# Optimization experiments

Hardware: AMD Instinct MI355X
Metric: run time of the kernel (lower is better)

Reference implementation:

```python
import jax, jax.numpy as jnp
from jax import lax
import numpy as np

PRE_NMS_TOPN = 2000
POST_NMS_TOPN = 300
NMS_IOU_THRESHOLD = 0.7
EPS = 1e-8


def setup_inputs() -> dict:
    key = jax.random.key(0)
    k1, k2 = jax.random.split(key, 2)
    B, H, W, A = 64, 100, 100, 9
    # small-magnitude deltas so exp(dh/dw) stays sane, as real RPN outputs do
    rpn_bbox_deltas = jax.random.normal(k1, (B, H, W, A * 4), dtype=jnp.float32) * 0.1
    rpn_labels = jax.random.uniform(k2, (B, H, W, A), dtype=jnp.float32)
    # grid anchors, normalized coords, 3 scales x 3 ratios = 9 per position
    ys = (jnp.arange(H, dtype=jnp.float32) + 0.5) / H
    xs = (jnp.arange(W, dtype=jnp.float32) + 0.5) / W
    scales = jnp.array([0.1, 0.2, 0.4], dtype=jnp.float32)
    ratios = jnp.array([0.5, 1.0, 2.0], dtype=jnp.float32)
    hh = (scales[:, None] * jnp.sqrt(ratios)[None, :]).reshape(-1)  # [9]
    ww = (scales[:, None] / jnp.sqrt(ratios)[None, :]).reshape(-1)  # [9]
    cy, cx = jnp.meshgrid(ys, xs, indexing="ij")  # [H,W]
    cy, cx = cy[..., None], cx[..., None]         # [H,W,1]
    anchors = jnp.stack(
        [cy - hh / 2, cx - ww / 2, cy + hh / 2, cx + ww / 2], axis=-1
    ).reshape(-1, 4)  # [H*W*9, 4] = [90000, 4]
    return {"rpn_bbox_deltas": rpn_bbox_deltas, "rpn_labels": rpn_labels, "anchors": anchors}


def _decode_deltas(anchors, deltas):
    # anchors [N,4] (y1,x1,y2,x2), deltas [B,N,4] (dy,dx,dh,dw)
    anc_h = anchors[:, 2] - anchors[:, 0]
    anc_w = anchors[:, 3] - anchors[:, 1]
    anc_cy = anchors[:, 0] + 0.5 * anc_h
    anc_cx = anchors[:, 1] + 0.5 * anc_w
    h = jnp.exp(deltas[..., 2]) * anc_h
    w = jnp.exp(deltas[..., 3]) * anc_w
    cy = deltas[..., 0] * anc_h + anc_cy
    cx = deltas[..., 1] * anc_w + anc_cx
    y1 = cy - 0.5 * h
    x1 = cx - 0.5 * w
    return jnp.stack([y1, x1, y1 + h, x1 + w], axis=-1)  # [B,N,4]


def _nms_single(boxes):
    # boxes [PRE,4] already sorted by score descending; greedy hard NMS
    n = boxes.shape[0]
    area = jnp.maximum(boxes[:, 2] - boxes[:, 0], 0.0) * jnp.maximum(boxes[:, 3] - boxes[:, 1], 0.0)
    idx = jnp.arange(n)

    def body(i, keep):
        b = boxes[i]
        yy1 = jnp.maximum(b[0], boxes[:, 0])
        xx1 = jnp.maximum(b[1], boxes[:, 1])
        yy2 = jnp.minimum(b[2], boxes[:, 2])
        xx2 = jnp.minimum(b[3], boxes[:, 3])
        inter = jnp.maximum(yy2 - yy1, 0.0) * jnp.maximum(xx2 - xx1, 0.0)
        iou = inter / (area[i] + area - inter + EPS)
        suppress = (iou > NMS_IOU_THRESHOLD) & (idx > i) & keep[i]
        return keep & ~suppress

    keep = lax.fori_loop(0, n, body, jnp.ones((n,), dtype=bool))
    # compact kept boxes (score order) into fixed [POST,4], zero-padded
    pos = jnp.where(keep, jnp.cumsum(keep) - 1, POST_NMS_TOPN)
    pos = jnp.minimum(pos, POST_NMS_TOPN)
    out = jnp.zeros((POST_NMS_TOPN + 1, 4), dtype=boxes.dtype).at[pos].set(boxes)[:POST_NMS_TOPN]
    return jnp.clip(out, 0.0, 1.0)  # clip_boxes=True in tf combined NMS


def reference(rpn_bbox_deltas, rpn_labels, anchors):
    B = rpn_bbox_deltas.shape[0]
    N = anchors.shape[0]
    deltas = rpn_bbox_deltas.reshape(B, N, 4)
    labels = rpn_labels.reshape(B, N)
    boxes = _decode_deltas(anchors, deltas)             # [B,N,4]
    _, pre_idx = lax.top_k(labels, PRE_NMS_TOPN)        # [B,PRE] sorted desc
    pre_boxes = jnp.take_along_axis(boxes, pre_idx[..., None], axis=1)  # [B,PRE,4]
    roi_bboxes = jax.vmap(_nms_single)(pre_boxes)       # [B,POST,4]
    return lax.stop_gradient(roi_bboxes)
```

## Files before the change

### kernel.cpp

```cpp
#include <hip/hip_runtime.h>
#include <stdint.h>


#define PRE 2000
#define POST 300
#define TILE 512
#define IOU_THR 0.7f
#define EPSV 1e-8f
#define SORTN 2048
#define NBINS 2048
#define CANDCAP 512
#define CONS 1984
#define SL 8
#define KBUF 1536

typedef unsigned long long u64;

__device__ __forceinline__ uint32_t flip_f32(uint32_t b) {
    return b ^ ((uint32_t)((int32_t)b >> 31) | 0x80000000u);
}

__device__ __forceinline__ int bin_of(float s) {
    int bn = (int)(s * 2048.0f);
    return min(max(bn, 0), NBINS - 1);
}

__device__ __forceinline__ u64 make_key(float s, int idx, int bn) {
    uint32_t ub = flip_f32(__float_as_uint(s));
    return ((u64)ub << 32) | ((uint32_t)bn << 20) |
           (uint32_t)(0xFFFFF - idx);
}

__device__ __forceinline__ bool iou_gt(const float4& bi, float ai,
                                       const float4& bj, float aj) {
    float yy1 = fmaxf(bi.x, bj.x);
    float xx1 = fmaxf(bi.y, bj.y);
    float yy2 = fminf(bi.z, bj.z);
    float xx2 = fminf(bi.w, bj.w);
    float inter = fmaxf(yy2 - yy1, 0.f) * fmaxf(xx2 - xx1, 0.f);
    float iou = inter / (ai + aj - inter + EPSV);
    return iou > IOU_THR;
}

__device__ __forceinline__ float area_of(const float4& bx) {
    return fmaxf(bx.z - bx.x, 0.f) * fmaxf(bx.w - bx.y, 0.f);
}

__device__ __forceinline__ u64 cs_keep(u64 v, u64 pv, int i, int j, int k) {
    bool lower   = ((i & j) == 0);
    bool desc    = ((i & k) == 0);
    bool keepmax = (desc == lower);
    u64 mx = v > pv ? v : pv;
    u64 mn = v > pv ? pv : v;
    return keepmax ? mx : mn;
}

__global__ __launch_bounds__(256) void k1_hist_gather(
    const float4* __restrict__ score4,
    uint32_t* __restrict__ g_hist,
    u64*      __restrict__ g_pairs,
    int*      __restrict__ g_scnt,
    int N)
{
    const int blk = blockIdx.x;
    const int b   = blk / SL;
    const int s   = blk % SL;
    const int tid = threadIdx.x;
    const int F4PB = N >> 2;
    const int F4PS = (F4PB + SL - 1) / SL;

    __shared__ uint32_t hist[NBINS];
    __shared__ u64 keybuf[KBUF];
    __shared__ int kcnt;

    for (int i = tid; i < NBINS; i += 256) hist[i] = 0u;
    if (tid == 0) kcnt = 0;
    __syncthreads();

    const float4* src = score4 + (size_t)b * F4PB;
    const int n0 = s * F4PS, n1 = min(n0 + F4PS, F4PB);
    for (int n = n0 + tid; n < n1; n += 256) {
        float4 v = src[n];
        float sv[4] = {v.x, v.y, v.z, v.w};
#pragma unroll
        for (int c = 0; c < 4; ++c) {
            int bn = bin_of(sv[c]);
            atomicAdd(&hist[bn], 1u);
            if (bn >= CONS) {
                int q = atomicAdd(&kcnt, 1);
                if (q < KBUF) keybuf[q] = make_key(sv[c], 4 * n + c, bn);
            }
        }
    }
    __syncthreads();

    uint32_t* gh = g_hist + ((size_t)b * SL + s) * NBINS;
    for (int i = tid; i < NBINS; i += 256) gh[i] = hist[i];

    if (tid == 0) g_scnt[b * SL + s] = kcnt;
    int lc = min(kcnt, KBUF);
    u64* gp = g_pairs + ((size_t)b * SL + s) * KBUF;
    for (int i = tid; i < lc; i += 256) gp[i] = keybuf[i];
}

__global__ __launch_bounds__(1024) void k2_sort(
    const float4* __restrict__ score4,
    const u64*  __restrict__ g_pairs,
    const int*  __restrict__ g_scnt,
    const uint32_t* __restrict__ g_hist,
    u64* __restrict__ g_sorted,
    int N)
{
    const int b    = blockIdx.x;
    const int tid  = threadIdx.x;
    const int lane = tid & 63;
    const int wv   = tid >> 6;

    __shared__ u64 pairs[SORTN];
    __shared__ u64 cand[CANDCAP];
    __shared__ uint32_t wtot[16];
    __shared__ int segbase[64];
    __shared__ int segcnt[64];
    __shared__ uint32_t cur[64];
    __shared__ int sh_bsel, sh_tprime, sh_cnt, sh_nc, sh_flag, sh_big;
    __shared__ uint32_t sh_pivot;

    const int F4PB = N >> 2;

    uint32_t* hist = (uint32_t*)pairs;
    {
        const uint32_t* gh = g_hist + (size_t)b * SL * NBINS;
#pragma unroll
        for (int h = 0; h < 2; ++h) {
            int i = tid + h * 1024;
            uint32_t acc = 0u;
#pragma unroll
            for (int s = 0; s < SL; ++s) acc += gh[(size_t)s * NBINS + i];
            hist[i] = acc;
        }
    }
    if (tid < 64) cur[tid] = 0u;
    if (tid == 0) {
        sh_cnt = 0; sh_nc = 0; sh_big = 0;
        int f = 0;
#pragma unroll
        for (int s = 0; s < SL; ++s)
            if (g_scnt[b * SL + s] > KBUF) f = 1;
        sh_flag = f;
    }
    __syncthreads();

    {
        const int i0 = wv * 128 + lane;
        const int i1 = i0 + 64;
        int h0 = (int)hist[i0];
        int h1 = (int)hist[i1];
        int s0 = h0, s1 = h1;
#pragma unroll
        for (int off = 1; off < 64; off <<= 1) {
            int t0 = __shfl_down(s0, off, 64);
            int t1 = __shfl_down(s1, off, 64);
            if (lane + off < 64) { s0 += t0; s1 += t1; }
        }
        int sum_h1 = __shfl(s1, 0, 64);
        if (lane == 0) wtot[wv] = (uint32_t)(__shfl(s0, 0, 64) + sum_h1);
        __syncthreads();
        int offtot = 0;
        for (int w2 = wv + 1; w2 < 16; ++w2) offtot += (int)wtot[w2];
        int S0 = s0 + sum_h1 + offtot;
        int S1 = s1 + offtot;
        if (S0 >= PRE && S0 - h0 < PRE) { sh_bsel = i0; sh_tprime = PRE - (S0 - h0); }
        if (S1 >= PRE && S1 - h1 < PRE) { sh_bsel = i1; sh_tprime = PRE - (S1 - h1); }
        if (i1 >= CONS) {
            segbase[i1 - CONS] = S1 - h1;
            segcnt [i1 - CONS] = h1;
        }
    }
    __syncthreads();
    const int bsel   = sh_bsel;
    const int tprime = sh_tprime;
    bool flag = (bsel < CONS) || sh_flag;
    if (!flag && segcnt[bsel - CONS] > CANDCAP) flag = true;
    __syncthreads();

    if (!flag) {
        for (int s = 0; s < SL; ++s) {
            const int  cs = min(g_scnt[b * SL + s], KBUF);
            const u64* gp = g_pairs + ((size_t)b * SL + s) * KBUF;
            for (int i = tid; i < cs; i += 1024) {
                u64 key = gp[i];
                int bn = (int)((key >> 20) & 0xFFFu);
                if (bn > bsel) {
                    int c = (int)atomicAdd(&cur[bn - CONS], 1u);
                    pairs[segbase[bn - CONS] + c] = key;
                } else if (bn == bsel) {
                    int t = atomicAdd(&sh_nc, 1);
                    if (t < CANDCAP) cand[t] = key;
                }
            }
        }
        __syncthreads();
        const int nc = min(sh_nc, CANDCAP);
        for (int i = tid; i < nc; i += 1024) {
            uint32_t vi = (uint32_t)(cand[i] >> 32);
            int g = 0, e = 0;
            for (int j = 0; j < nc; ++j) {
                uint32_t vj = (uint32_t)(cand[j] >> 32);
                g += (vj > vi);
                e += (vj == vi);
            }
            if (g < tprime && g + e >= tprime) sh_pivot = vi;
        }
        __syncthreads();
        const uint32_t pivot = sh_pivot;
        for (int i = tid; i < nc; i += 1024) {
            uint32_t vi = (uint32_t)(cand[i] >> 32);
            if (vi >= pivot) {
                int c = (int)atomicAdd(&cur[bsel - CONS], 1u);
                pairs[segbase[bsel - CONS] + c] = cand[i];
            }
        }
        __syncthreads();
        const int total = segbase[bsel - CONS] + (int)cur[bsel - CONS];
        for (int q = total + tid; q < SORTN; q += 1024) pairs[q] = 0ull;
        if (tid < 64 && (int)cur[tid] > 128) sh_big = 1;
        __syncthreads();
    } else {
        const float4* src = score4 + (size_t)b * F4PB;
        for (int n = tid; n < F4PB; n += 1024) {
            float4 v = src[n];
            float sv[4] = {v.x, v.y, v.z, v.w};
#pragma unroll
            for (int c = 0; c < 4; ++c) {
                int bn = bin_of(sv[c]);
                if (bn >= bsel) {
                    u64 key = make_key(sv[c], 4 * n + c, bn);
                    if (bn > bsel) {
                        int q = atomicAdd(&sh_cnt, 1);
                        if (q < SORTN) pairs[q] = key;
                    } else {
                        int t = atomicAdd(&sh_nc, 1);
                        if (t < CANDCAP) cand[t] = key;
                    }
                }
            }
        }
        __syncthreads();
        const int nc = min(sh_nc, CANDCAP);
        for (int i = tid; i < nc; i += 1024) {
            uint32_t vi = (uint32_t)(cand[i] >> 32);
            int g = 0, e = 0;
            for (int j = 0; j < nc; ++j) {
                uint32_t vj = (uint32_t)(cand[j] >> 32);
                g += (vj > vi);
                e += (vj == vi);
            }
            if (g < tprime && g + e >= tprime) sh_pivot = vi;
        }
        __syncthreads();
        const uint32_t pivot = sh_pivot;
        for (int i = tid; i < nc; i += 1024) {
            uint32_t vi = (uint32_t)(cand[i] >> 32);
            if (vi >= pivot) {
                int q = atomicAdd(&sh_cnt, 1);
                if (q < SORTN) pairs[q] = cand[i];
            }
        }
        __syncthreads();
        const int total = min(sh_cnt, SORTN);
        for (int q = total + tid; q < SORTN; q += 1024) pairs[q] = 0ull;
        if (tid == 0) sh_big = 1;
        __syncthreads();
    }

    if (!sh_big) {
        for (int sgi = wv; sgi < 64; sgi += 16) {
            int n = (int)cur[sgi];
            if (n <= 0) continue;
            int base = segbase[sgi];
            if (n <= 64) {
                u64 e = (lane < n) ? pairs[base + lane] : 0ull;
#pragma unroll
                for (int k = 2; k <= 64; k <<= 1)
                    for (int j = k >> 1; j > 0; j >>= 1)
                        e = cs_keep(e, __shfl_xor(e, j, 64), lane, j, k);
                if (lane < n) pairs[base + lane] = e;
            } else {
                u64 e0 = (lane < n) ? pairs[base + lane] : 0ull;
                u64 e1 = (lane + 64 < n) ? pairs[base + lane + 64] : 0ull;
#pragma unroll
                for (int k = 2; k <= 128; k <<= 1) {
                    for (int j = k >> 1; j > 0; j >>= 1) {
                        if (j == 64) {
                            u64 a = e0, c = e1;
                            e0 = cs_keep(a, c, lane, 64, k);
                            e1 = cs_keep(c, a, lane + 64, 64, k);
                        } else {
                            e0 = cs_keep(e0, __shfl_xor(e0, j, 64), lane, j, k);
                            e1 = cs_keep(e1, __shfl_xor(e1, j, 64), lane + 64, j, k);
                        }
                    }
                }
                if (lane < n) pairs[base + lane] = e0;
                if (lane + 64 < n) pairs[base + lane + 64] = e1;
            }
        }
        __syncthreads();
        g_sorted[(size_t)b * SORTN + tid]        = pairs[tid];
        g_sorted[(size_t)b * SORTN + tid + 1024] = pairs[tid + 1024];
    } else {
        const int i0 = wv * 128 + lane;
        const int i1 = i0 + 64;
        u64 e0 = pairs[i0];
        u64 e1 = pairs[i1];
        for (int k = 2; k <= SORTN; k <<= 1) {
            for (int j = k >> 1; j > 0; j >>= 1) {
                if (j >= 128) {
                    pairs[i0] = e0;
                    pairs[i1] = e1;
                    __syncthreads();
                    u64 p0 = pairs[i0 ^ j];
                    u64 p1 = pairs[i1 ^ j];
                    __syncthreads();
                    e0 = cs_keep(e0, p0, i0, j, k);
                    e1 = cs_keep(e1, p1, i1, j, k);
                } else if (j == 64) {
                    u64 a = e0, c = e1;
                    e0 = cs_keep(a, c, i0, 64, k);
                    e1 = cs_keep(c, a, i1, 64, k);
                } else {
                    e0 = cs_keep(e0, __shfl_xor(e0, j, 64), i0, j, k);
                    e1 = cs_keep(e1, __shfl_xor(e1, j, 64), i1, j, k);
                }
            }
        }
        g_sorted[(size_t)b * SORTN + i0] = e0;
        g_sorted[(size_t)b * SORTN + i1] = e1;
    }
}

__global__ __launch_bounds__(256) void k3_decode(
    const float4* __restrict__ deltas,
    const float4* __restrict__ anchors,
    const u64*  __restrict__ g_sorted,
    float4* __restrict__ g_boxes,
    float*  __restrict__ g_area,
    int N)
{
    const int b   = blockIdx.x >> 2;
    const int s   = blockIdx.x & 3;
    const int tid = threadIdx.x;
    const int r0 = s * 512, r1 = min(r0 + 512, PRE);

    const float4* dl = deltas + (size_t)b * N;
    for (int r = r0 + tid; r < r1; r += 256) {
        u64 key = g_sorted[(size_t)b * SORTN + r];
        uint32_t idx = 0xFFFFFu - (uint32_t)(key & 0xFFFFFull);
        float4 bx = make_float4(0.f, 0.f, 0.f, 0.f);
        float  ar = 0.f;
        if (idx < (uint32_t)N) {
            float4 d  = dl[idx];
            float4 an = anchors[idx];
            float ah  = an.z - an.x;
            float aw  = an.w - an.y;
            float acy = an.x + 0.5f * ah;
            float acx = an.y + 0.5f * aw;
            float h   = expf(d.z) * ah;
            float w   = expf(d.w) * aw;
            float cy  = d.x * ah + acy;
            float cx  = d.y * aw + acx;
            float y1  = cy - 0.5f * h;
            float x1  = cx - 0.5f * w;
            bx = make_float4(y1, x1, y1 + h, x1 + w);
            ar = fmaxf(bx.z - bx.x, 0.f) * fmaxf(bx.w - bx.y, 0.f);
        }
        g_boxes[(size_t)b * PRE + r] = bx;
        g_area [(size_t)b * PRE + r] = ar;
    }
}

__global__ __launch_bounds__(256) void k4_supmat(
    const float4* __restrict__ g_boxes,
    uint32_t* __restrict__ g_supmat,
    uint32_t* __restrict__ g_supT)
{
    const int b   = blockIdx.x >> 4;
    const int s   = blockIdx.x & 15;
    const int tid = threadIdx.x;

    __shared__ float4 box[TILE];
    for (int i = tid; i < TILE; i += 256)
        box[i] = g_boxes[(size_t)b * PRE + i];
    __syncthreads();

    const int rbase = s * 32;
#pragma unroll
    for (int k = 0; k < 2; ++k) {
        int idx = tid + k * 256;
        int row = rbase + (idx & 31);
        int w   = idx >> 5;
        int jbase = w << 5;
        float4 bi = box[row];
        float  ai = area_of(bi);
        uint32_t bits = 0u;
        if (jbase + 31 > row) {
#pragma unroll
            for (int c = 0; c < 32; ++c) {
                int j = jbase + c;
                float4 bj = box[j];
                float  aj = area_of(bj);
                bool gt = (j > row) & iou_gt(bi, ai, bj, aj);
                bits |= ((uint32_t)gt) << c;
            }
        }
        g_supmat[((size_t)b * TILE + row) * 16 + w] = bits;
    }

    if (s < 8 && tid < 128) {
        int q  = s;
        int j  = tid >> 1;
        int w2 = tid & 1;
        int C  = q * 64 + j;
        float4 bc = box[C];
        float  ac = area_of(bc);
        uint32_t bits = 0u;
#pragma unroll
        for (int c = 0; c < 32; ++c) {
            int R = q * 64 + w2 * 32 + c;
            float4 br = box[R];
            float  ar = area_of(br);
            bool gt = (R < C) & iou_gt(br, ar, bc, ac);
            bits |= ((uint32_t)gt) << c;
        }
        g_supT[((size_t)b * TILE + C) * 2 + w2] = bits;
    }
}

__global__ __launch_bounds__(64) void k5_sweep(
    const uint32_t* __restrict__ g_supmat,
    const u64*    __restrict__ g_supT64,
    const float4* __restrict__ g_boxes,
    const float*  __restrict__ g_area,
    float4* __restrict__ out)
{
    const int b    = blockIdx.x;
    const int lane = threadIdx.x;

    __shared__ uint32_t kept[POST];
    __shared__ u64 sh_keepbits[TILE / 64];
    __shared__ uint32_t fmask[(PRE - TILE + 31) / 32];
    __shared__ int sh_kc;

    const u64* tdbase = g_supT64 + (size_t)b * TILE;

    uint32_t removedw = 0u;
    int kc = 0, nq = 0;
    u64 cw_cur = tdbase[lane];
    for (int q = 0; q < TILE / 64; ++q) {
        u64 cw_next = (q < TILE / 64 - 1) ? tdbase[(q + 1) * 64 + lane] : 0ull;
        const int cbase = q << 6;
        uint32_t rlo = (uint32_t)__builtin_amdgcn_readlane((int)removedw, 2 * q);
        uint32_t rhi = (uint32_t)__builtin_amdgcn_readlane((int)removedw, 2 * q + 1);
        u64 avail = ~(((u64)rhi << 32) | rlo);
        u64 K = 0ull;
        while (avail) {
            int i = __ffsll((long long)avail) - 1;
            K |= (1ull << i);
            u64 supp = __ballot(((cw_cur >> i) & 1ull) != 0ull);
            avail &= ~(supp | (1ull << i));
        }
        if (lane == 0) sh_keepbits[q] = K;
        kc += __popcll(K);
        nq = q + 1;
        if (kc >= POST) break;
        if (K) {
            const int w = lane & 15;
            const int g = lane >> 4;
            const uint32_t* gs =
                g_supmat + ((size_t)b * TILE + cbase + g * 16) * 16 + w;
            uint32_t acc = 0u;
#pragma unroll
            for (int r = 0; r < 16; ++r)
                if ((K >> (g * 16 + r)) & 1ull) acc |= gs[(size_t)r * 16];
            acc |= (uint32_t)__shfl_xor((int)acc, 16, 64);
            acc |= (uint32_t)__shfl_xor((int)acc, 32, 64);
            if (lane < 16) removedw |= acc;
        }
        cw_cur = cw_next;
    }
    {
        int base = 0;
        for (int q = 0; q < nq; ++q) {
            u64 kbq = sh_keepbits[q];
            int pos = base + __popcll(kbq & ((1ull << lane) - 1));
            if (((kbq >> lane) & 1ull) && pos < POST)
                kept[pos] = (uint32_t)(q * 64 + lane);
            base += __popcll(kbq);
        }
        if (lane == 0) sh_kc = min(kc, POST);
    }
    __syncthreads();
    int kcf = sh_kc;

    if (kcf < POST) {
        for (int w = lane; w < (PRE - TILE + 31) / 32; w += 64) fmask[w] = 0u;
        __syncthreads();
        for (int j = TILE + lane; j < PRE; j += 64) {
            float4 bj = g_boxes[(size_t)b * PRE + j];
            float  aj = g_area [(size_t)b * PRE + j];
            bool supd = false;
            for (int k = 0; k < kcf; ++k) {
                int i = (int)kept[k];
                float4 bi = g_boxes[(size_t)b * PRE + i];
                float  ai = g_area [(size_t)b * PRE + i];
                if (iou_gt(bi, ai, bj, aj)) { supd = true; break; }
            }
            if (supd) atomicOr(&fmask[(j - TILE) >> 5], 1u << ((j - TILE) & 31));
        }
        __syncthreads();
        int i = TILE;
        while (i < PRE && kcf < POST) {
            while (i < PRE && ((fmask[(i - TILE) >> 5] >> ((i - TILE) & 31)) & 1u)) ++i;
            if (i >= PRE) break;
            if (lane == 0) kept[kcf] = (uint32_t)i;
            ++kcf;
            if (kcf >= POST) break;
            float4 bi = g_boxes[(size_t)b * PRE + i];
            float  ai = g_area [(size_t)b * PRE + i];
            for (int j = i + 1 + lane; j < PRE; j += 64) {
                float4 bj = g_boxes[(size_t)b * PRE + j];
                float  aj = g_area [(size_t)b * PRE + j];
                if (iou_gt(bi, ai, bj, aj))
                    atomicOr(&fmask[(j - TILE) >> 5], 1u << ((j - TILE) & 31));
            }
            ++i;
            __syncthreads();
        }
    }
    __syncthreads();

    float4* ob = out + (size_t)b * POST;
    for (int r = lane; r < POST; r += 64) {
        float4 o = make_float4(0.f, 0.f, 0.f, 0.f);
        if (r < kcf) {
            float4 bx = g_boxes[(size_t)b * PRE + kept[r]];
            o.x = fminf(fmaxf(bx.x, 0.f), 1.f);
            o.y = fminf(fmaxf(bx.y, 0.f), 1.f);
            o.z = fminf(fmaxf(bx.z, 0.f), 1.f);
            o.w = fminf(fmaxf(bx.w, 0.f), 1.f);
        }
        ob[r] = o;
    }
}

extern "C" void kernel_launch(void* const* d_in, const int* in_sizes, int n_in,
                              void* d_out, int out_size, void* d_ws, size_t ws_size,
                              hipStream_t stream) {
    const float4* deltas  = (const float4*)d_in[0];
    const float*  labels  = (const float*)d_in[1];
    const float4* anchors = (const float4*)d_in[2];
    const float4* score4  = (const float4*)labels;
    float4*       outp    = (float4*)d_out;
    const int N = in_sizes[2] / 4;
    const int B = in_sizes[1] / N;

    char* ws = (char*)d_ws;
    const size_t SZ_BOXES  = (size_t)B * PRE * 16;
    const size_t SZ_PAIRS  = (size_t)B * SL * KBUF * 8;
    const size_t SZ_SORTED = (size_t)B * SORTN * 8;
    const size_t SZ_SUPMAT = (size_t)B * TILE * 16 * 4;
    const size_t SZ_SUPT   = (size_t)B * TILE * 8;
    const size_t SZ_AREA   = (size_t)B * PRE * 4;
    const size_t SZ_HIST   = (size_t)B * SL * NBINS * 4;
    float4*   g_boxes  = (float4*)ws;
    u64*      g_pairs  = (u64*)(ws + SZ_BOXES);
    u64*      g_sorted = (u64*)(ws + SZ_BOXES + SZ_PAIRS);
    uint32_t* g_supmat = (uint32_t*)(ws + SZ_BOXES + SZ_PAIRS + SZ_SORTED);
    uint32_t* g_supT   = (uint32_t*)(ws + SZ_BOXES + SZ_PAIRS + SZ_SORTED + SZ_SUPMAT);
    float*    g_area   = (float*)(ws + SZ_BOXES + SZ_PAIRS + SZ_SORTED + SZ_SUPMAT + SZ_SUPT);
    uint32_t* g_hist   = (uint32_t*)(ws + SZ_BOXES + SZ_PAIRS + SZ_SORTED + SZ_SUPMAT + SZ_SUPT + SZ_AREA);
    int*      g_scnt   = (int*)((char*)g_hist + SZ_HIST);

    k1_hist_gather<<<B * SL, 256, 0, stream>>>(score4, g_hist, g_pairs,
                                               g_scnt, N);
    k2_sort<<<B, 1024, 0, stream>>>(score4, g_pairs, g_scnt, g_hist,
                                    g_sorted, N);
    k3_decode<<<B * 4, 256, 0, stream>>>(deltas, anchors, g_sorted,
                                         g_boxes, g_area, N);
    k4_supmat<<<B * 16, 256, 0, stream>>>(g_boxes, g_supmat, g_supT);
    k5_sweep<<<B, 64, 0, stream>>>(g_supmat, (const u64*)g_supT,
                                   g_boxes, g_area, outp);
}
```

Measured before the change: 93.06 us.

## Fuse decode and diagonal suppression tiles into sort kernel, drop global histograms

Stops building the full 2048-bin histogram in the gather kernel and instead builds a 64-bin histogram from the gathered top-bin keys inside the sort kernel. All keys in the top bins are sorted by segment (total up to 4096), and a full histogram with rescan is kept only as a fallback. Box decode and the diagonal-block transposed suppression bits are fused into the sort kernel through shared memory, which removes one launch and the g_sorted and g_hist global round trips. The gather now uses more slices with smaller buffers. The trade-off is more shared memory and work in a single 1024-thread block per batch, which runs only 64 blocks.

```diff
diff --git a/kernel.cpp b/kernel.cpp
--- a/kernel.cpp
+++ b/kernel.cpp
@@ -9,10 +9,11 @@
 #define EPSV 1e-8f
 #define SORTN 2048
 #define NBINS 2048
+#define DESTCAP 4096
 #define CANDCAP 512
 #define CONS 1984
-#define SL 8
-#define KBUF 1536
+#define SL 16
+#define KBUF 768
 
 typedef unsigned long long u64;
 
@@ -55,11 +56,10 @@
     return keepmax ? mx : mn;
 }
 
-__global__ __launch_bounds__(256) void k1_hist_gather(
+__global__ __launch_bounds__(256) void k1_gather(
     const float4* __restrict__ score4,
-    uint32_t* __restrict__ g_hist,
-    u64*      __restrict__ g_pairs,
-    int*      __restrict__ g_scnt,
+    u64* __restrict__ g_pairs,
+    int* __restrict__ g_scnt,
     int N)
 {
     const int blk = blockIdx.x;
@@ -69,11 +69,9 @@
     const int F4PB = N >> 2;
     const int F4PS = (F4PB + SL - 1) / SL;
 
-    __shared__ uint32_t hist[NBINS];
     __shared__ u64 keybuf[KBUF];
     __shared__ int kcnt;
 
-    for (int i = tid; i < NBINS; i += 256) hist[i] = 0u;
     if (tid == 0) kcnt = 0;
     __syncthreads();
 
@@ -85,7 +83,6 @@
 #pragma unroll
         for (int c = 0; c < 4; ++c) {
             int bn = bin_of(sv[c]);
-            atomicAdd(&hist[bn], 1u);
             if (bn >= CONS) {
                 int q = atomicAdd(&kcnt, 1);
                 if (q < KBUF) keybuf[q] = make_key(sv[c], 4 * n + c, bn);
@@ -93,9 +90,6 @@
         }
     }
     __syncthreads();
-
-    uint32_t* gh = g_hist + ((size_t)b * SL + s) * NBINS;
-    for (int i = tid; i < NBINS; i += 256) gh[i] = hist[i];
 
     if (tid == 0) g_scnt[b * SL + s] = kcnt;
     int lc = min(kcnt, KBUF);
@@ -107,8 +101,11 @@
     const float4* __restrict__ score4,
     const u64*  __restrict__ g_pairs,
     const int*  __restrict__ g_scnt,
-    const uint32_t* __restrict__ g_hist,
-    u64* __restrict__ g_sorted,
+    const float4* __restrict__ deltas,
+    const float4* __restrict__ anchors,
+    float4* __restrict__ g_boxes,
+    float*  __restrict__ g_area,
+    uint32_t* __restrict__ g_supT,
     int N)
 {
     const int b    = blockIdx.x;
@@ -116,178 +113,78 @@
     const int lane = tid & 63;
     const int wv   = tid >> 6;
 
-    __shared__ u64 pairs[SORTN];
+    __shared__ u64 dest[DESTCAP];
+    __shared__ float4 sbox[TILE];
     __shared__ u64 cand[CANDCAP];
+    __shared__ uint32_t hist64[64];
+    __shared__ int segbase64[64];
+    __shared__ uint32_t cur64[64];
+    __shared__ int scnt_s[SL];
     __shared__ uint32_t wtot[16];
-    __shared__ int segbase[64];
-    __shared__ int segcnt[64];
-    __shared__ uint32_t cur[64];
-    __shared__ int sh_bsel, sh_tprime, sh_cnt, sh_nc, sh_flag, sh_big;
+    __shared__ int sh_flag, sh_total, sh_bsel, sh_tprime, sh_cnt, sh_nc;
     __shared__ uint32_t sh_pivot;
 
     const int F4PB = N >> 2;
 
-    uint32_t* hist = (uint32_t*)pairs;
+    if (tid < SL) scnt_s[tid] = g_scnt[b * SL + tid];
+    if (tid < 64) { hist64[tid] = 0u; cur64[tid] = 0u; }
+    if (tid == 0) { sh_flag = 0; sh_cnt = 0; sh_nc = 0; }
+    __syncthreads();
+
     {
-        const uint32_t* gh = g_hist + (size_t)b * SL * NBINS;
-#pragma unroll
-        for (int h = 0; h < 2; ++h) {
-            int i = tid + h * 1024;
-            uint32_t acc = 0u;
-#pragma unroll
-            for (int s = 0; s < SL; ++s) acc += gh[(size_t)s * NBINS + i];
-            hist[i] = acc;
-        }
-    }
-    if (tid < 64) cur[tid] = 0u;
-    if (tid == 0) {
-        sh_cnt = 0; sh_nc = 0; sh_big = 0;
-        int f = 0;
-#pragma unroll
-        for (int s = 0; s < SL; ++s)
-            if (g_scnt[b * SL + s] > KBUF) f = 1;
-        sh_flag = f;
-    }
-    __syncthreads();
-
-    {
-        const int i0 = wv * 128 + lane;
-        const int i1 = i0 + 64;
-        int h0 = (int)hist[i0];
-        int h1 = (int)hist[i1];
-        int s0 = h0, s1 = h1;
+        int raw = scnt_s[wv];
+        if (raw > KBUF) sh_flag = 1;
+        int cs = min(raw, KBUF);
+        const u64* gp = g_pairs + ((size_t)b * SL + wv) * KBUF;
+        for (int i = lane; i < cs; i += 64) {
+            int b64 = (int)((gp[i] >> 20) & 0xFFFu) - CONS;
+            atomicAdd(&hist64[b64], 1u);
+        }
+    }
+    __syncthreads();
+
+    if (wv == 0) {
+        int h = (int)hist64[lane];
+        int ssum = h;
 #pragma unroll
         for (int off = 1; off < 64; off <<= 1) {
-            int t0 = __shfl_down(s0, off, 64);
-            int t1 = __shfl_down(s1, off, 64);
-            if (lane + off < 64) { s0 += t0; s1 += t1; }
-        }
-        int sum_h1 = __shfl(s1, 0, 64);
-        if (lane == 0) wtot[wv] = (uint32_t)(__shfl(s0, 0, 64) + sum_h1);
-        __syncthreads();
-        int offtot = 0;
-        for (int w2 = wv + 1; w2 < 16; ++w2) offtot += (int)wtot[w2];
-        int S0 = s0 + sum_h1 + offtot;
-        int S1 = s1 + offtot;
-        if (S0 >= PRE && S0 - h0 < PRE) { sh_bsel = i0; sh_tprime = PRE - (S0 - h0); }
-        if (S1 >= PRE && S1 - h1 < PRE) { sh_bsel = i1; sh_tprime = PRE - (S1 - h1); }
-        if (i1 >= CONS) {
-            segbase[i1 - CONS] = S1 - h1;
-            segcnt [i1 - CONS] = h1;
-        }
-    }
-    __syncthreads();
-    const int bsel   = sh_bsel;
-    const int tprime = sh_tprime;
-    bool flag = (bsel < CONS) || sh_flag;
-    if (!flag && segcnt[bsel - CONS] > CANDCAP) flag = true;
-    __syncthreads();
+            int t = __shfl_down(ssum, off, 64);
+            if (lane + off < 64) ssum += t;
+        }
+        segbase64[lane] = ssum - h;
+        if (lane == 0) sh_total = ssum;
+        if (h > 128) sh_flag = 1;
+    }
+    __syncthreads();
+    const int total = sh_total;
+    if (tid == 0 && (total < PRE || total > DESTCAP)) sh_flag = 1;
+    __syncthreads();
+    const bool flag = (sh_flag != 0);
 
     if (!flag) {
-        for (int s = 0; s < SL; ++s) {
-            const int  cs = min(g_scnt[b * SL + s], KBUF);
-            const u64* gp = g_pairs + ((size_t)b * SL + s) * KBUF;
-            for (int i = tid; i < cs; i += 1024) {
-                u64 key = gp[i];
-                int bn = (int)((key >> 20) & 0xFFFu);
-                if (bn > bsel) {
-                    int c = (int)atomicAdd(&cur[bn - CONS], 1u);
-                    pairs[segbase[bn - CONS] + c] = key;
-                } else if (bn == bsel) {
-                    int t = atomicAdd(&sh_nc, 1);
-                    if (t < CANDCAP) cand[t] = key;
-                }
-            }
-        }
-        __syncthreads();
-        const int nc = min(sh_nc, CANDCAP);
-        for (int i = tid; i < nc; i += 1024) {
-            uint32_t vi = (uint32_t)(cand[i] >> 32);
-            int g = 0, e = 0;
-            for (int j = 0; j < nc; ++j) {
-                uint32_t vj = (uint32_t)(cand[j] >> 32);
-                g += (vj > vi);
-                e += (vj == vi);
-            }
-            if (g < tprime && g + e >= tprime) sh_pivot = vi;
-        }
-        __syncthreads();
-        const uint32_t pivot = sh_pivot;
-        for (int i = tid; i < nc; i += 1024) {
-            uint32_t vi = (uint32_t)(cand[i] >> 32);
-            if (vi >= pivot) {
-                int c = (int)atomicAdd(&cur[bsel - CONS], 1u);
-                pairs[segbase[bsel - CONS] + c] = cand[i];
-            }
-        }
-        __syncthreads();
-        const int total = segbase[bsel - CONS] + (int)cur[bsel - CONS];
-        for (int q = total + tid; q < SORTN; q += 1024) pairs[q] = 0ull;
-        if (tid < 64 && (int)cur[tid] > 128) sh_big = 1;
-        __syncthreads();
-    } else {
-        const float4* src = score4 + (size_t)b * F4PB;
-        for (int n = tid; n < F4PB; n += 1024) {
-            float4 v = src[n];
-            float sv[4] = {v.x, v.y, v.z, v.w};
-#pragma unroll
-            for (int c = 0; c < 4; ++c) {
-                int bn = bin_of(sv[c]);
-                if (bn >= bsel) {
-                    u64 key = make_key(sv[c], 4 * n + c, bn);
-                    if (bn > bsel) {
-                        int q = atomicAdd(&sh_cnt, 1);
-                        if (q < SORTN) pairs[q] = key;
-                    } else {
-                        int t = atomicAdd(&sh_nc, 1);
-                        if (t < CANDCAP) cand[t] = key;
-                    }
-                }
-            }
-        }
-        __syncthreads();
-        const int nc = min(sh_nc, CANDCAP);
-        for (int i = tid; i < nc; i += 1024) {
-            uint32_t vi = (uint32_t)(cand[i] >> 32);
-            int g = 0, e = 0;
-            for (int j = 0; j < nc; ++j) {
-                uint32_t vj = (uint32_t)(cand[j] >> 32);
-                g += (vj > vi);
-                e += (vj == vi);
-            }
-            if (g < tprime && g + e >= tprime) sh_pivot = vi;
-        }
-        __syncthreads();
-        const uint32_t pivot = sh_pivot;
-        for (int i = tid; i < nc; i += 1024) {
-            uint32_t vi = (uint32_t)(cand[i] >> 32);
-            if (vi >= pivot) {
-                int q = atomicAdd(&sh_cnt, 1);
-                if (q < SORTN) pairs[q] = cand[i];
-            }
-        }
-        __syncthreads();
-        const int total = min(sh_cnt, SORTN);
-        for (int q = total + tid; q < SORTN; q += 1024) pairs[q] = 0ull;
-        if (tid == 0) sh_big = 1;
-        __syncthreads();
-    }
-
-    if (!sh_big) {
+        int cs = min(scnt_s[wv], KBUF);
+        const u64* gp = g_pairs + ((size_t)b * SL + wv) * KBUF;
+        for (int i = lane; i < cs; i += 64) {
+            u64 key = gp[i];
+            int b64 = (int)((key >> 20) & 0xFFFu) - CONS;
+            int c = (int)atomicAdd(&cur64[b64], 1u);
+            dest[segbase64[b64] + c] = key;
+        }
+        __syncthreads();
         for (int sgi = wv; sgi < 64; sgi += 16) {
-            int n = (int)cur[sgi];
+            int n = (int)cur64[sgi];
             if (n <= 0) continue;
-            int base = segbase[sgi];
+            int base = segbase64[sgi];
             if (n <= 64) {
-                u64 e = (lane < n) ? pairs[base + lane] : 0ull;
+                u64 e = (lane < n) ? dest[base + lane] : 0ull;
 #pragma unroll
                 for (int k = 2; k <= 64; k <<= 1)
                     for (int j = k >> 1; j > 0; j >>= 1)
                         e = cs_keep(e, __shfl_xor(e, j, 64), lane, j, k);
-                if (lane < n) pairs[base + lane] = e;
+                if (lane < n) dest[base + lane] = e;
             } else {
-                u64 e0 = (lane < n) ? pairs[base + lane] : 0ull;
-                u64 e1 = (lane + 64 < n) ? pairs[base + lane + 64] : 0ull;
+                u64 e0 = (lane < n) ? dest[base + lane] : 0ull;
+                u64 e1 = (lane + 64 < n) ? dest[base + lane + 64] : 0ull;
 #pragma unroll
                 for (int k = 2; k <= 128; k <<= 1) {
                     for (int j = k >> 1; j > 0; j >>= 1) {
@@ -301,60 +198,129 @@
                         }
                     }
                 }
-                if (lane < n) pairs[base + lane] = e0;
-                if (lane + 64 < n) pairs[base + lane + 64] = e1;
-            }
-        }
-        __syncthreads();
-        g_sorted[(size_t)b * SORTN + tid]        = pairs[tid];
-        g_sorted[(size_t)b * SORTN + tid + 1024] = pairs[tid + 1024];
+                if (lane < n) dest[base + lane] = e0;
+                if (lane + 64 < n) dest[base + lane + 64] = e1;
+            }
+        }
+        __syncthreads();
     } else {
-        const int i0 = wv * 128 + lane;
-        const int i1 = i0 + 64;
-        u64 e0 = pairs[i0];
-        u64 e1 = pairs[i1];
-        for (int k = 2; k <= SORTN; k <<= 1) {
-            for (int j = k >> 1; j > 0; j >>= 1) {
-                if (j >= 128) {
-                    pairs[i0] = e0;
-                    pairs[i1] = e1;
-                    __syncthreads();
-                    u64 p0 = pairs[i0 ^ j];
-                    u64 p1 = pairs[i1 ^ j];
-                    __syncthreads();
-                    e0 = cs_keep(e0, p0, i0, j, k);
-                    e1 = cs_keep(e1, p1, i1, j, k);
-                } else if (j == 64) {
-                    u64 a = e0, c = e1;
-                    e0 = cs_keep(a, c, i0, 64, k);
-                    e1 = cs_keep(c, a, i1, 64, k);
-                } else {
-                    e0 = cs_keep(e0, __shfl_xor(e0, j, 64), i0, j, k);
-                    e1 = cs_keep(e1, __shfl_xor(e1, j, 64), i1, j, k);
+        uint32_t* hist = (uint32_t*)sbox;
+        hist[tid] = 0u; hist[tid + 1024] = 0u;
+        if (tid == 0) { sh_cnt = 0; sh_nc = 0; }
+        __syncthreads();
+        const float4* src = score4 + (size_t)b * F4PB;
+        for (int n = tid; n < F4PB; n += 1024) {
+            float4 v = src[n];
+            atomicAdd(&hist[bin_of(v.x)], 1u);
+            atomicAdd(&hist[bin_of(v.y)], 1u);
+            atomicAdd(&hist[bin_of(v.z)], 1u);
+            atomicAdd(&hist[bin_of(v.w)], 1u);
+        }
+        __syncthreads();
+        {
+            const int i0 = wv * 128 + lane;
+            const int i1 = i0 + 64;
+            int h0 = (int)hist[i0];
+            int h1 = (int)hist[i1];
+            int s0 = h0, s1 = h1;
+#pragma unroll
+            for (int off = 1; off < 64; off <<= 1) {
+                int t0 = __shfl_down(s0, off, 64);
+                int t1 = __shfl_down(s1, off, 64);
+                if (lane + off < 64) { s0 += t0; s1 += t1; }
+            }
+            int sum_h1 = __shfl(s1, 0, 64);
+            if (lane == 0) wtot[wv] = (uint32_t)(__shfl(s0, 0, 64) + sum_h1);
+            __syncthreads();
+            int offtot = 0;
+            for (int w2 = wv + 1; w2 < 16; ++w2) offtot += (int)wtot[w2];
+            int S0 = s0 + sum_h1 + offtot;
+            int S1 = s1 + offtot;
+            if (S0 >= PRE && S0 - h0 < PRE) { sh_bsel = i0; sh_tprime = PRE - (S0 - h0); }
+            if (S1 >= PRE && S1 - h1 < PRE) { sh_bsel = i1; sh_tprime = PRE - (S1 - h1); }
+        }
+        __syncthreads();
+        const int bsel   = sh_bsel;
+        const int tprime = sh_tprime;
+        __syncthreads();
+        for (int n = tid; n < F4PB; n += 1024) {
+            float4 v = src[n];
+            float sv[4] = {v.x, v.y, v.z, v.w};
+#pragma unroll
+            for (int c = 0; c < 4; ++c) {
+                int bn = bin_of(sv[c]);
+                if (bn >= bsel) {
+                    u64 key = make_key(sv[c], 4 * n + c, bn);
+                    if (bn > bsel) {
+                        int q = atomicAdd(&sh_cnt, 1);
+                        if (q < SORTN) dest[q] = key;
+                    } else {
+                        int t = atomicAdd(&sh_nc, 1);
+                        if (t < CANDCAP) cand[t] = key;
+                    }
                 }
             }
         }
-        g_sorted[(size_t)b * SORTN + i0] = e0;
-        g_sorted[(size_t)b * SORTN + i1] = e1;
-    }
-}
-
-__global__ __launch_bounds__(256) void k3_decode(
-    const float4* __restrict__ deltas,
-    const float4* __restrict__ anchors,
-    const u64*  __restrict__ g_sorted,
-    float4* __restrict__ g_boxes,
-    float*  __restrict__ g_area,
-    int N)
-{
-    const int b   = blockIdx.x >> 2;
-    const int s   = blockIdx.x & 3;
-    const int tid = threadIdx.x;
-    const int r0 = s * 512, r1 = min(r0 + 512, PRE);
+        __syncthreads();
+        const int nc = min(sh_nc, CANDCAP);
+        for (int i = tid; i < nc; i += 1024) {
+            uint32_t vi = (uint32_t)(cand[i] >> 32);
+            int g = 0, e = 0;
+            for (int j = 0; j < nc; ++j) {
+                uint32_t vj = (uint32_t)(cand[j] >> 32);
+                g += (vj > vi);
+                e += (vj == vi);
+            }
+            if (g < tprime && g + e >= tprime) sh_pivot = vi;
+        }
+        __syncthreads();
+        const uint32_t pivot = sh_pivot;
+        for (int i = tid; i < nc; i += 1024) {
+            uint32_t vi = (uint32_t)(cand[i] >> 32);
+            if (vi >= pivot) {
+                int q = atomicAdd(&sh_cnt, 1);
+                if (q < SORTN) dest[q] = cand[i];
+            }
+        }
+        __syncthreads();
+        const int tt = min(sh_cnt, SORTN);
+        for (int q = tt + tid; q < SORTN; q += 1024) dest[q] = 0ull;
+        __syncthreads();
+        {
+            const int i0 = wv * 128 + lane;
+            const int i1 = i0 + 64;
+            u64 e0 = dest[i0];
+            u64 e1 = dest[i1];
+            for (int k = 2; k <= SORTN; k <<= 1) {
+                for (int j = k >> 1; j > 0; j >>= 1) {
+                    if (j >= 128) {
+                        dest[i0] = e0;
+                        dest[i1] = e1;
+                        __syncthreads();
+                        u64 p0 = dest[i0 ^ j];
+                        u64 p1 = dest[i1 ^ j];
+                        __syncthreads();
+                        e0 = cs_keep(e0, p0, i0, j, k);
+                        e1 = cs_keep(e1, p1, i1, j, k);
+                    } else if (j == 64) {
+                        u64 a = e0, c = e1;
+                        e0 = cs_keep(a, c, i0, 64, k);
+                        e1 = cs_keep(c, a, i1, 64, k);
+                    } else {
+                        e0 = cs_keep(e0, __shfl_xor(e0, j, 64), i0, j, k);
+                        e1 = cs_keep(e1, __shfl_xor(e1, j, 64), i1, j, k);
+                    }
+                }
+            }
+            dest[i0] = e0;
+            dest[i1] = e1;
+        }
+        __syncthreads();
+    }
 
     const float4* dl = deltas + (size_t)b * N;
-    for (int r = r0 + tid; r < r1; r += 256) {
-        u64 key = g_sorted[(size_t)b * SORTN + r];
+    for (int r = tid; r < PRE; r += 1024) {
+        u64 key = dest[r];
         uint32_t idx = 0xFFFFFu - (uint32_t)(key & 0xFFFFFull);
         float4 bx = make_float4(0.f, 0.f, 0.f, 0.f);
         float  ar = 0.f;
@@ -376,13 +342,33 @@
         }
         g_boxes[(size_t)b * PRE + r] = bx;
         g_area [(size_t)b * PRE + r] = ar;
+        if (r < TILE) sbox[r] = bx;
+    }
+    __syncthreads();
+
+    {
+        int q  = tid >> 7;
+        int j  = (tid >> 1) & 63;
+        int w2 = tid & 1;
+        int C  = q * 64 + j;
+        float4 bc = sbox[C];
+        float  ac = area_of(bc);
+        uint32_t bits = 0u;
+#pragma unroll
+        for (int c = 0; c < 32; ++c) {
+            int R = q * 64 + w2 * 32 + c;
+            float4 br = sbox[R];
+            float  ar = area_of(br);
+            bool gt = (R < C) & iou_gt(br, ar, bc, ac);
+            bits |= ((uint32_t)gt) << c;
+        }
+        g_supT[((size_t)b * TILE + C) * 2 + w2] = bits;
     }
 }
 
 __global__ __launch_bounds__(256) void k4_supmat(
     const float4* __restrict__ g_boxes,
-    uint32_t* __restrict__ g_supmat,
-    uint32_t* __restrict__ g_supT)
+    uint32_t* __restrict__ g_supmat)
 {
     const int b   = blockIdx.x >> 4;
     const int s   = blockIdx.x & 15;
@@ -414,25 +400,6 @@
             }
         }
         g_supmat[((size_t)b * TILE + row) * 16 + w] = bits;
-    }
-
-    if (s < 8 && tid < 128) {
-        int q  = s;
-        int j  = tid >> 1;
-        int w2 = tid & 1;
-        int C  = q * 64 + j;
-        float4 bc = box[C];
-        float  ac = area_of(bc);
-        uint32_t bits = 0u;
-#pragma unroll
-        for (int c = 0; c < 32; ++c) {
-            int R = q * 64 + w2 * 32 + c;
-            float4 br = box[R];
-            float  ar = area_of(br);
-            bool gt = (R < C) & iou_gt(br, ar, bc, ac);
-            bits |= ((uint32_t)gt) << c;
-        }
-        g_supT[((size_t)b * TILE + C) * 2 + w2] = bits;
     }
 }
 
@@ -567,27 +534,20 @@
     char* ws = (char*)d_ws;
     const size_t SZ_BOXES  = (size_t)B * PRE * 16;
     const size_t SZ_PAIRS  = (size_t)B * SL * KBUF * 8;
-    const size_t SZ_SORTED = (size_t)B * SORTN * 8;
     const size_t SZ_SUPMAT = (size_t)B * TILE * 16 * 4;
     const size_t SZ_SUPT   = (size_t)B * TILE * 8;
     const size_t SZ_AREA   = (size_t)B * PRE * 4;
-    const size_t SZ_HIST   = (size_t)B * SL * NBINS * 4;
     float4*   g_boxes  = (float4*)ws;
     u64*      g_pairs  = (u64*)(ws + SZ_BOXES);
-    u64*      g_sorted = (u64*)(ws + SZ_BOXES + SZ_PAIRS);
-    uint32_t* g_supmat = (uint32_t*)(ws + SZ_BOXES + SZ_PAIRS + SZ_SORTED);
-    uint32_t* g_supT   = (uint32_t*)(ws + SZ_BOXES + SZ_PAIRS + SZ_SORTED + SZ_SUPMAT);
-    float*    g_area   = (float*)(ws + SZ_BOXES + SZ_PAIRS + SZ_SORTED + SZ_SUPMAT + SZ_SUPT);
-    uint32_t* g_hist   = (uint32_t*)(ws + SZ_BOXES + SZ_PAIRS + SZ_SORTED + SZ_SUPMAT + SZ_SUPT + SZ_AREA);
-    int*      g_scnt   = (int*)((char*)g_hist + SZ_HIST);
-
-    k1_hist_gather<<<B * SL, 256, 0, stream>>>(score4, g_hist, g_pairs,
-                                               g_scnt, N);
-    k2_sort<<<B, 1024, 0, stream>>>(score4, g_pairs, g_scnt, g_hist,
-                                    g_sorted, N);
-    k3_decode<<<B * 4, 256, 0, stream>>>(deltas, anchors, g_sorted,
-                                         g_boxes, g_area, N);
-    k4_supmat<<<B * 16, 256, 0, stream>>>(g_boxes, g_supmat, g_supT);
+    uint32_t* g_supmat = (uint32_t*)(ws + SZ_BOXES + SZ_PAIRS);
+    uint32_t* g_supT   = (uint32_t*)(ws + SZ_BOXES + SZ_PAIRS + SZ_SUPMAT);
+    float*    g_area   = (float*)(ws + SZ_BOXES + SZ_PAIRS + SZ_SUPMAT + SZ_SUPT);
+    int*      g_scnt   = (int*)(ws + SZ_BOXES + SZ_PAIRS + SZ_SUPMAT + SZ_SUPT + SZ_AREA);
+
+    k1_gather<<<B * SL, 256, 0, stream>>>(score4, g_pairs, g_scnt, N);
+    k2_sort<<<B, 1024, 0, stream>>>(score4, g_pairs, g_scnt, deltas, anchors,
+                                    g_boxes, g_area, g_supT, N);
+    k4_supmat<<<B * 16, 256, 0, stream>>>(g_boxes, g_supmat);
     k5_sweep<<<B, 64, 0, stream>>>(g_supmat, (const u64*)g_supT,
                                    g_boxes, g_area, outp);
 }
```

New measurement: 88.40 us. 1.05x faster.
